# Optimization experiments

Measured on AMD Instinct MI355X. Metric: run time of the kernel, lower is better.

Reference implementation:

```python
import jax, jax.numpy as jnp
import numpy as np

NUM_HEADS = 8

def _spectral_normalize(w, u):
    # One power iteration (power_iterations=1), as in the TF wrapper.
    w2 = w.reshape(-1, w.shape[-1])            # [in, out]
    v = u @ w2.T                               # [1, in]
    v = v / jnp.linalg.norm(v)
    u_new = v @ w2                             # [1, out]
    u_new = u_new / jnp.linalg.norm(u_new)
    sigma = (v @ w2) @ u_new.T                 # [1,1]
    # TF applies normalization by variable assignment (no grad through sigma)
    return w / jax.lax.stop_gradient(sigma[0, 0])

def setup_inputs() -> dict:
    key = jax.random.key(0)
    ks = jax.random.split(key, 14)
    F = 1024
    def dense(k1, k2, k3):
        w = jax.random.normal(k1, (F, F), jnp.float32) * (1.0 / np.sqrt(F))
        b = jnp.zeros((F,), jnp.float32)
        u = jax.random.normal(k3, (1, F), jnp.float32) * 0.02
        return w, b, u
    wq, bq, uq = dense(ks[0], ks[1], ks[2])
    wk, bk, uk = dense(ks[3], ks[4], ks[5])
    wv, bv, uv = dense(ks[6], ks[7], ks[8])
    wo, bo, uo = dense(ks[9], ks[10], ks[11])
    x = jax.random.normal(ks[12], (4, 2048, F), jnp.float32)
    gamma = jnp.array(1.0, jnp.float32)
    return {"x": x, "wq": wq, "bq": bq, "uq": uq, "wk": wk, "bk": bk, "uk": uk,
            "wv": wv, "bv": bv, "uv": uv, "wo": wo, "bo": bo, "uo": uo, "gamma": gamma}

def reference(x, wq, bq, uq, wk, bk, uk, wv, bv, uv, wo, bo, uo, gamma):
    B, S, F = x.shape
    D = F // NUM_HEADS
    def proj(w, b, u):
        return x @ _spectral_normalize(w, u) + b
    def split_heads(t):
        return t.reshape(B, S, NUM_HEADS, D).transpose(0, 2, 1, 3)  # [B,H,S,D]
    q = split_heads(proj(wq, bq, uq))
    k = split_heads(proj(wk, bk, uk))
    v = split_heads(proj(wv, bv, uv))
    # NOTE: original has no 1/sqrt(depth) scaling -- faithful to source.
    logits = jnp.einsum('bhsd,bhtd->bhst', q, k)          # [B,H,S,S]
    attn = jax.nn.softmax(logits, axis=-1)
    ctx = jnp.einsum('bhst,bhtd->bhsd', attn, v)           # [B,H,S,D]
    concat = ctx.transpose(0, 2, 1, 3).reshape(B, S, F)    # merge heads
    # Dropout omitted (deterministic reference / inference mode).
    out = x + (concat @ _spectral_normalize(wo, uo) + bo) * gamma
    return (out, attn)
```

## Files before the change

kernel.cpp:

```cpp
#include <hip/hip_runtime.h>
#include <math.h>

typedef _Float16 h16;
typedef _Float16 half8 __attribute__((ext_vector_type(8)));
typedef _Float16 half4 __attribute__((ext_vector_type(4)));
typedef float floatx4 __attribute__((ext_vector_type(4)));

#define MFMA16(a, b, c) __builtin_amdgcn_mfma_f32_16x16x32_f16(a, b, c, 0, 0, 0)

__global__ void sigma_s1(const float* __restrict__ w0, const float* __restrict__ w1,
                         const float* __restrict__ w2, const float* __restrict__ w3,
                         const float* __restrict__ u0, const float* __restrict__ u1,
                         const float* __restrict__ u2, const float* __restrict__ u3,
                         float* __restrict__ tvec, float* __restrict__ acc) {
    int m = blockIdx.y;
    const float* w = (m == 0) ? w0 : (m == 1) ? w1 : (m == 2) ? w2 : w3;
    const float* u = (m == 0) ? u0 : (m == 1) ? u1 : (m == 2) ? u2 : u3;
    int wid = threadIdx.x >> 6, lane = threadIdx.x & 63;
    int row = blockIdx.x * 4 + wid;
    const float* wr = w + row * 1024;
    float s = 0.f;
    for (int k = 0; k < 16; k++) { int j = lane + 64 * k; s += u[j] * wr[j]; }
    for (int off = 32; off; off >>= 1) s += __shfl_xor(s, off, 64);
    if (lane == 0) { tvec[m * 1024 + row] = s; atomicAdd(acc + m * 2, s * s); }
}

__global__ void sigma_s2(const float* __restrict__ w0, const float* __restrict__ w1,
                         const float* __restrict__ w2, const float* __restrict__ w3,
                         const float* __restrict__ tvec, float* __restrict__ acc) {
    int m = blockIdx.y;
    const float* w = (m == 0) ? w0 : (m == 1) ? w1 : (m == 2) ? w2 : w3;
    const float* t = tvec + m * 1024;
    int j = blockIdx.x * 256 + threadIdx.x;
    float z = 0.f;
    for (int i = 0; i < 1024; i++) z += t[i] * w[i * 1024 + j];
    z = z * z;
    for (int off = 32; off; off >>= 1) z += __shfl_xor(z, off, 64);
    __shared__ float red[4];
    int wid = threadIdx.x >> 6, lane = threadIdx.x & 63;
    if (lane == 0) red[wid] = z;
    __syncthreads();
    if (threadIdx.x == 0) atomicAdd(acc + m * 2 + 1, red[0] + red[1] + red[2] + red[3]);
}

__global__ void sigma_s3(const float* __restrict__ acc, float* __restrict__ inv_sigma) {
    int m = threadIdx.x;
    if (m < 4) inv_sigma[m] = sqrtf(acc[m * 2] / acc[m * 2 + 1]);
}

__global__ void prep_w(const float* __restrict__ w, const float* __restrict__ inv_sigma,
                       int midx, h16* __restrict__ whT, h16* __restrict__ wlT) {
    __shared__ float tile[32][33];
    float is = inv_sigma[midx];
    int i0 = blockIdx.x * 32, j0 = blockIdx.y * 32;
    int tx = threadIdx.x, ty = threadIdx.y;
    for (int r = 0; r < 32; r += 8)
        tile[r + ty][tx] = w[(i0 + r + ty) * 1024 + j0 + tx] * is;
    __syncthreads();
    for (int r = 0; r < 32; r += 8) {
        int j = j0 + r + ty, i = i0 + tx;
        float v = tile[tx][r + ty];
        h16 h = (h16)v;
        whT[j * 1024 + i] = h;
        wlT[j * 1024 + i] = (h16)(v - (float)h);
    }
}

__global__ void prep_x(const float4* __restrict__ x4, half4* __restrict__ xh,
                       half4* __restrict__ xl) {
    int i = blockIdx.x * 256 + threadIdx.x;
    float4 v = x4[i];
    float a[4] = {v.x, v.y, v.z, v.w};
    half4 h, l;
    for (int k = 0; k < 4; k++) {
        h16 hh = (h16)a[k];
        h[k] = hh;
        l[k] = (h16)(a[k] - (float)hh);
    }
    xh[i] = h;
    xl[i] = l;
}

template <int SPLIT>
__global__ __launch_bounds__(256, 2) void gemm_proj(
    const h16* __restrict__ Ah_g, const h16* __restrict__ Al_g,
    const h16* __restrict__ Bh_g, const h16* __restrict__ Bl_g,
    const float* __restrict__ bias, h16* __restrict__ outh, h16* __restrict__ outl) {
    __shared__ h16 As[2][128 * 40];
    __shared__ h16 Bs[2][128 * 40];
    int tid = threadIdx.x;
    int m0 = blockIdx.y * 128, n0 = blockIdx.x * 128;
    int wid = tid >> 6, lane = tid & 63;
    int wm = (wid >> 1) * 64, wn = (wid & 1) * 64;
    int lrow = lane & 15, quad = lane >> 4;
    floatx4 acc[4][4] = {};
    for (int kt = 0; kt < 1024; kt += 32) {
        for (int i = 0; i < 2; i++) {
            int c = tid + 256 * i;
            int row = c >> 2, col = (c & 3) * 8;
            *(half8*)&As[0][row * 40 + col] = *(const half8*)&Ah_g[(m0 + row) * 1024 + kt + col];
            *(half8*)&Bs[0][row * 40 + col] = *(const half8*)&Bh_g[(n0 + row) * 1024 + kt + col];
            if (SPLIT) {
                *(half8*)&As[1][row * 40 + col] = *(const half8*)&Al_g[(m0 + row) * 1024 + kt + col];
                *(half8*)&Bs[1][row * 40 + col] = *(const half8*)&Bl_g[(n0 + row) * 1024 + kt + col];
            }
        }
        __syncthreads();
        half8 a_h[4], a_l[4], b_h[4], b_l[4];
        for (int f = 0; f < 4; f++) {
            a_h[f] = *(const half8*)&As[0][(wm + f * 16 + lrow) * 40 + quad * 8];
            b_h[f] = *(const half8*)&Bs[0][(wn + f * 16 + lrow) * 40 + quad * 8];
            if (SPLIT) {
                a_l[f] = *(const half8*)&As[1][(wm + f * 16 + lrow) * 40 + quad * 8];
                b_l[f] = *(const half8*)&Bs[1][(wn + f * 16 + lrow) * 40 + quad * 8];
            }
        }
        for (int mf = 0; mf < 4; mf++)
            for (int nf = 0; nf < 4; nf++) {
                acc[mf][nf] = MFMA16(a_h[mf], b_h[nf], acc[mf][nf]);
                if (SPLIT) {
                    acc[mf][nf] = MFMA16(a_h[mf], b_l[nf], acc[mf][nf]);
                    acc[mf][nf] = MFMA16(a_l[mf], b_h[nf], acc[mf][nf]);
                }
            }
        __syncthreads();
    }
    for (int nf = 0; nf < 4; nf++) {
        int n = n0 + wn + nf * 16 + lrow;
        float b = bias[n];
        int h = n >> 7, d = n & 127;
        for (int mf = 0; mf < 4; mf++)
            for (int r = 0; r < 4; r++) {
                int mg = m0 + wm + mf * 16 + quad * 4 + r;
                int bb = mg >> 11, s = mg & 2047;
                int idx = ((bb * 8 + h) * 2048 + s) * 128 + d;
                float v = acc[mf][nf][r] + b;
                h16 hh = (h16)v;
                outh[idx] = hh;
                if (SPLIT) outl[idx] = (h16)(v - (float)hh);
            }
    }
}

__global__ void transpose_v(const h16* __restrict__ vh, h16* __restrict__ vT) {
    __shared__ h16 tile[32][33];
    int bh = blockIdx.z;
    int t0 = blockIdx.x * 32, d0 = blockIdx.y * 32;
    int tx = threadIdx.x, ty = threadIdx.y;
    const h16* src = vh + bh * 2048 * 128;
    h16* dst = vT + bh * 128 * 2048;
    for (int r = 0; r < 32; r += 8) tile[r + ty][tx] = src[(t0 + r + ty) * 128 + d0 + tx];
    __syncthreads();
    for (int r = 0; r < 32; r += 8) dst[(d0 + r + ty) * 2048 + t0 + tx] = tile[tx][r + ty];
}

__global__ __launch_bounds__(256, 2) void gemm_logits(
    const h16* __restrict__ qh, const h16* __restrict__ ql,
    const h16* __restrict__ kh, const h16* __restrict__ kl, float* __restrict__ attn) {
    __shared__ h16 As[2][128 * 40];
    __shared__ h16 Bs[2][128 * 40];
    int tid = threadIdx.x;
    int bh = blockIdx.z;
    int s0 = blockIdx.y * 128, t0 = blockIdx.x * 128;
    const h16* Ah_g = qh + bh * 2048 * 128;
    const h16* Al_g = ql + bh * 2048 * 128;
    const h16* Bh_g = kh + bh * 2048 * 128;
    const h16* Bl_g = kl + bh * 2048 * 128;
    int wid = tid >> 6, lane = tid & 63;
    int wm = (wid >> 1) * 64, wn = (wid & 1) * 64;
    int lrow = lane & 15, quad = lane >> 4;
    floatx4 acc[4][4] = {};
    for (int kt = 0; kt < 128; kt += 32) {
        for (int i = 0; i < 2; i++) {
            int c = tid + 256 * i;
            int row = c >> 2, col = (c & 3) * 8;
            *(half8*)&As[0][row * 40 + col] = *(const half8*)&Ah_g[(s0 + row) * 128 + kt + col];
            *(half8*)&As[1][row * 40 + col] = *(const half8*)&Al_g[(s0 + row) * 128 + kt + col];
            *(half8*)&Bs[0][row * 40 + col] = *(const half8*)&Bh_g[(t0 + row) * 128 + kt + col];
            *(half8*)&Bs[1][row * 40 + col] = *(const half8*)&Bl_g[(t0 + row) * 128 + kt + col];
        }
        __syncthreads();
        half8 a_h[4], a_l[4], b_h[4], b_l[4];
        for (int f = 0; f < 4; f++) {
            a_h[f] = *(const half8*)&As[0][(wm + f * 16 + lrow) * 40 + quad * 8];
            a_l[f] = *(const half8*)&As[1][(wm + f * 16 + lrow) * 40 + quad * 8];
            b_h[f] = *(const half8*)&Bs[0][(wn + f * 16 + lrow) * 40 + quad * 8];
            b_l[f] = *(const half8*)&Bs[1][(wn + f * 16 + lrow) * 40 + quad * 8];
        }
        for (int mf = 0; mf < 4; mf++)
            for (int nf = 0; nf < 4; nf++) {
                acc[mf][nf] = MFMA16(a_h[mf], b_h[nf], acc[mf][nf]);
                acc[mf][nf] = MFMA16(a_h[mf], b_l[nf], acc[mf][nf]);
                acc[mf][nf] = MFMA16(a_l[mf], b_h[nf], acc[mf][nf]);
            }
        __syncthreads();
    }
    for (int nf = 0; nf < 4; nf++) {
        int t = t0 + wn + nf * 16 + lrow;
        for (int mf = 0; mf < 4; mf++)
            for (int r = 0; r < 4; r++) {
                int s = s0 + wm + mf * 16 + quad * 4 + r;
                attn[(bh * 2048 + s) * 2048 + t] = acc[mf][nf][r];
            }
    }
}

__global__ void row_stats(const float* __restrict__ attn, float* __restrict__ m_arr,
                          float* __restrict__ z_arr) {
    int wid = threadIdx.x >> 6, lane = threadIdx.x & 63;
    int r = blockIdx.x * 4 + wid;
    const float4* row = (const float4*)(attn + (size_t)r * 2048);
    float4 v[8];
    float mx = -1e30f;
    for (int i = 0; i < 8; i++) {
        v[i] = row[i * 64 + lane];
        mx = fmaxf(mx, fmaxf(fmaxf(v[i].x, v[i].y), fmaxf(v[i].z, v[i].w)));
    }
    for (int off = 32; off; off >>= 1) mx = fmaxf(mx, __shfl_xor(mx, off, 64));
    float z = 0.f;
    for (int i = 0; i < 8; i++)
        z += __expf(v[i].x - mx) + __expf(v[i].y - mx) + __expf(v[i].z - mx) + __expf(v[i].w - mx);
    for (int off = 32; off; off >>= 1) z += __shfl_xor(z, off, 64);
    if (lane == 0) { m_arr[r] = mx; z_arr[r] = z; }
}

__global__ __launch_bounds__(256, 2) void gemm_pv(
    float* __restrict__ attn, const h16* __restrict__ vT, const float* __restrict__ m_arr,
    const float* __restrict__ z_arr, h16* __restrict__ ctx) {
    __shared__ h16 Ps[128 * 72];
    __shared__ h16 Vs[128 * 72];
    __shared__ float ms[128], izs[128];
    int tid = threadIdx.x;
    int bh = blockIdx.y, s0 = blockIdx.x * 128;
    if (tid < 128) ms[tid] = m_arr[bh * 2048 + s0 + tid];
    else izs[tid - 128] = 1.f / z_arr[bh * 2048 + s0 + tid - 128];
    __syncthreads();
    int wid = tid >> 6, lane = tid & 63;
    int wm = (wid >> 1) * 64, wn = (wid & 1) * 64;
    int lrow = lane & 15, quad = lane >> 4;
    float* attn_b = attn + ((size_t)bh * 2048 + s0) * 2048;
    const h16* vT_b = vT + bh * 128 * 2048;
    floatx4 acc[4][4] = {};
    for (int t0 = 0; t0 < 2048; t0 += 64) {
        for (int i = 0; i < 8; i++) {
            int c = tid + 256 * i;
            int row = c >> 4, c4 = c & 15;
            float4* p = (float4*)&attn_b[(size_t)row * 2048 + t0 + c4 * 4];
            float4 l = *p;
            float mm = ms[row], iz = izs[row];
            float4 e;
            e.x = __expf(l.x - mm) * iz;
            e.y = __expf(l.y - mm) * iz;
            e.z = __expf(l.z - mm) * iz;
            e.w = __expf(l.w - mm) * iz;
            *p = e;
            half4 ph;
            ph[0] = (h16)e.x; ph[1] = (h16)e.y; ph[2] = (h16)e.z; ph[3] = (h16)e.w;
            *(half4*)&Ps[row * 72 + c4 * 4] = ph;
        }
        for (int i = 0; i < 4; i++) {
            int c = tid + 256 * i;
            int row = c >> 3, c8 = (c & 7) * 8;
            *(half8*)&Vs[row * 72 + c8] = *(const half8*)&vT_b[row * 2048 + t0 + c8];
        }
        __syncthreads();
        for (int ks = 0; ks < 2; ks++) {
            half8 a[4], b[4];
            for (int f = 0; f < 4; f++) {
                a[f] = *(const half8*)&Ps[(wm + f * 16 + lrow) * 72 + ks * 32 + quad * 8];
                b[f] = *(const half8*)&Vs[(wn + f * 16 + lrow) * 72 + ks * 32 + quad * 8];
            }
            for (int mf = 0; mf < 4; mf++)
                for (int nf = 0; nf < 4; nf++)
                    acc[mf][nf] = MFMA16(a[mf], b[nf], acc[mf][nf]);
        }
        __syncthreads();
    }
    int b = bh >> 3, h = bh & 7;
    for (int nf = 0; nf < 4; nf++) {
        int d = wn + nf * 16 + lrow;
        for (int mf = 0; mf < 4; mf++)
            for (int r = 0; r < 4; r++) {
                int s = s0 + wm + mf * 16 + quad * 4 + r;
                ctx[(b * 2048 + s) * 1024 + h * 128 + d] = (h16)acc[mf][nf][r];
            }
    }
}

__global__ __launch_bounds__(256, 2) void gemm_out(
    const h16* __restrict__ Ah_g, const h16* __restrict__ Bh_g, const float* __restrict__ bo,
    const float* __restrict__ x, const float* __restrict__ gamma_p, float* __restrict__ out) {
    __shared__ h16 As[128 * 40];
    __shared__ h16 Bs[128 * 40];
    int tid = threadIdx.x;
    int m0 = blockIdx.y * 128, n0 = blockIdx.x * 128;
    int wid = tid >> 6, lane = tid & 63;
    int wm = (wid >> 1) * 64, wn = (wid & 1) * 64;
    int lrow = lane & 15, quad = lane >> 4;
    floatx4 acc[4][4] = {};
    for (int kt = 0; kt < 1024; kt += 32) {
        for (int i = 0; i < 2; i++) {
            int c = tid + 256 * i;
            int row = c >> 2, col = (c & 3) * 8;
            *(half8*)&As[row * 40 + col] = *(const half8*)&Ah_g[(m0 + row) * 1024 + kt + col];
            *(half8*)&Bs[row * 40 + col] = *(const half8*)&Bh_g[(n0 + row) * 1024 + kt + col];
        }
        __syncthreads();
        half8 a[4], b[4];
        for (int f = 0; f < 4; f++) {
            a[f] = *(const half8*)&As[(wm + f * 16 + lrow) * 40 + quad * 8];
            b[f] = *(const half8*)&Bs[(wn + f * 16 + lrow) * 40 + quad * 8];
        }
        for (int mf = 0; mf < 4; mf++)
            for (int nf = 0; nf < 4; nf++)
                acc[mf][nf] = MFMA16(a[mf], b[nf], acc[mf][nf]);
        __syncthreads();
    }
    float g = *gamma_p;
    for (int nf = 0; nf < 4; nf++) {
        int n = n0 + wn + nf * 16 + lrow;
        float bb = bo[n];
        for (int mf = 0; mf < 4; mf++)
            for (int r = 0; r < 4; r++) {
                int mg = m0 + wm + mf * 16 + quad * 4 + r;
                out[mg * 1024 + n] = x[mg * 1024 + n] + (acc[mf][nf][r] + bb) * g;
            }
    }
}

extern "C" void kernel_launch(void* const* d_in, const int* in_sizes, int n_in,
                              void* d_out, int out_size, void* d_ws, size_t ws_size,
                              hipStream_t stream) {
    const float* x = (const float*)d_in[0];
    const float* wq = (const float*)d_in[1];
    const float* bq = (const float*)d_in[2];
    const float* uq = (const float*)d_in[3];
    const float* wk = (const float*)d_in[4];
    const float* bk = (const float*)d_in[5];
    const float* uk = (const float*)d_in[6];
    const float* wv = (const float*)d_in[7];
    const float* bv = (const float*)d_in[8];
    const float* uv = (const float*)d_in[9];
    const float* wo = (const float*)d_in[10];
    const float* bo = (const float*)d_in[11];
    const float* uo = (const float*)d_in[12];
    const float* gamma = (const float*)d_in[13];
    float* out_f = (float*)d_out;
    float* attn = out_f + 8388608;

    char* ws = (char*)d_ws;
    size_t o = 0;
    auto alloc = [&](size_t b) { size_t r = o; o += (b + 255) & ~(size_t)255; return r; };
    const size_t SZ_X = (size_t)8192 * 1024 * 2;
    const size_t SZ_W = (size_t)1024 * 1024 * 2;
    const size_t SZ_Q = (size_t)32 * 2048 * 128 * 2;
    h16* xh = (h16*)(ws + alloc(SZ_X));
    h16* xl = (h16*)(ws + alloc(SZ_X));
    h16* wqhT = (h16*)(ws + alloc(SZ_W));
    h16* wqlT = (h16*)(ws + alloc(SZ_W));
    h16* wkhT = (h16*)(ws + alloc(SZ_W));
    h16* wklT = (h16*)(ws + alloc(SZ_W));
    h16* wvhT = (h16*)(ws + alloc(SZ_W));
    h16* wvlT = (h16*)(ws + alloc(SZ_W));
    h16* wohT = (h16*)(ws + alloc(SZ_W));
    h16* wolT = (h16*)(ws + alloc(SZ_W));
    h16* qh = (h16*)(ws + alloc(SZ_Q));
    h16* ql = (h16*)(ws + alloc(SZ_Q));
    h16* kh = (h16*)(ws + alloc(SZ_Q));
    h16* kl = (h16*)(ws + alloc(SZ_Q));
    h16* vh = (h16*)(ws + alloc(SZ_Q));
    h16* vT = (h16*)(ws + alloc(SZ_Q));
    h16* ctx = (h16*)(ws + alloc(SZ_Q));
    float* tvec = (float*)(ws + alloc(4096 * 4));
    float* sacc = (float*)(ws + alloc(8 * 4));
    float* isig = (float*)(ws + alloc(4 * 4));
    float* m_arr = (float*)(ws + alloc(65536 * 4));
    float* z_arr = (float*)(ws + alloc(65536 * 4));

    (void)hipMemsetAsync(sacc, 0, 8 * 4, stream);
    sigma_s1<<<dim3(256, 4), 256, 0, stream>>>(wq, wk, wv, wo, uq, uk, uv, uo, tvec, sacc);
    sigma_s2<<<dim3(4, 4), 256, 0, stream>>>(wq, wk, wv, wo, tvec, sacc);
    sigma_s3<<<1, 64, 0, stream>>>(sacc, isig);

    prep_w<<<dim3(32, 32), dim3(32, 8), 0, stream>>>(wq, isig, 0, wqhT, wqlT);
    prep_w<<<dim3(32, 32), dim3(32, 8), 0, stream>>>(wk, isig, 1, wkhT, wklT);
    prep_w<<<dim3(32, 32), dim3(32, 8), 0, stream>>>(wv, isig, 2, wvhT, wvlT);
    prep_w<<<dim3(32, 32), dim3(32, 8), 0, stream>>>(wo, isig, 3, wohT, wolT);
    prep_x<<<8192, 256, 0, stream>>>((const float4*)x, (half4*)xh, (half4*)xl);

    gemm_proj<1><<<dim3(8, 64), 256, 0, stream>>>(xh, xl, wqhT, wqlT, bq, qh, ql);
    gemm_proj<1><<<dim3(8, 64), 256, 0, stream>>>(xh, xl, wkhT, wklT, bk, kh, kl);
    gemm_proj<0><<<dim3(8, 64), 256, 0, stream>>>(xh, xl, wvhT, wvlT, bv, vh, nullptr);
    transpose_v<<<dim3(64, 4, 32), dim3(32, 8), 0, stream>>>(vh, vT);

    gemm_logits<<<dim3(16, 16, 32), 256, 0, stream>>>(qh, ql, kh, kl, attn);
    row_stats<<<16384, 256, 0, stream>>>(attn, m_arr, z_arr);
    gemm_pv<<<dim3(16, 32), 256, 0, stream>>>(attn, vT, m_arr, z_arr, ctx);
    gemm_out<<<dim3(8, 64), 256, 0, stream>>>(ctx, wohT, bo, x, gamma, out_f);

    (void)in_sizes; (void)n_in; (void)out_size; (void)ws_size;
}
```

Baseline: 1.597 ms.

## Fuse softmax row statistics into logits GEMM and load GEMM tiles directly to LDS

The logits GEMM epilogue now computes a per-row partial max and sum-of-exponentials for each 64-column tile and writes them to scratch. A small combine kernel then merges these partials into the final row max and normaliser, replacing the separate row_stats pass that re-read the full fp32 attention matrix. Separately, all GEMM kernels switch from register-staged global-to-LDS copies to global_load_lds 16-byte direct loads. This drops the padded LDS row stride of 40, so the fragment reads may hit more LDS bank conflicts. The partial-stat buffers reuse the ctx workspace before gemm_pv writes it.

```diff
diff --git a/kernel.cpp b/kernel.cpp
--- a/kernel.cpp
+++ b/kernel.cpp
@@ -7,6 +7,11 @@
 typedef float floatx4 __attribute__((ext_vector_type(4)));
 
 #define MFMA16(a, b, c) __builtin_amdgcn_mfma_f32_16x16x32_f16(a, b, c, 0, 0, 0)
+
+__device__ __forceinline__ void gload16(const void* g, void* l) {
+    __builtin_amdgcn_global_load_lds((const __attribute__((address_space(1))) unsigned int*)g,
+                                     (__attribute__((address_space(3))) unsigned int*)l, 16, 0, 0);
+}
 
 __global__ void sigma_s1(const float* __restrict__ w0, const float* __restrict__ w1,
                          const float* __restrict__ w2, const float* __restrict__ w3,
@@ -86,33 +91,35 @@
     const h16* __restrict__ Ah_g, const h16* __restrict__ Al_g,
     const h16* __restrict__ Bh_g, const h16* __restrict__ Bl_g,
     const float* __restrict__ bias, h16* __restrict__ outh, h16* __restrict__ outl) {
-    __shared__ h16 As[2][128 * 40];
-    __shared__ h16 Bs[2][128 * 40];
+    __shared__ h16 As[2][128 * 32];
+    __shared__ h16 Bs[2][128 * 32];
     int tid = threadIdx.x;
     int m0 = blockIdx.y * 128, n0 = blockIdx.x * 128;
     int wid = tid >> 6, lane = tid & 63;
     int wm = (wid >> 1) * 64, wn = (wid & 1) * 64;
     int lrow = lane & 15, quad = lane >> 4;
+    int srow = lane >> 2;
+    int scol = (lane & 3) * 8;
     floatx4 acc[4][4] = {};
     for (int kt = 0; kt < 1024; kt += 32) {
-        for (int i = 0; i < 2; i++) {
-            int c = tid + 256 * i;
-            int row = c >> 2, col = (c & 3) * 8;
-            *(half8*)&As[0][row * 40 + col] = *(const half8*)&Ah_g[(m0 + row) * 1024 + kt + col];
-            *(half8*)&Bs[0][row * 40 + col] = *(const half8*)&Bh_g[(n0 + row) * 1024 + kt + col];
+        for (int j = 0; j < 2; j++) {
+            int rb = j * 64 + wid * 16;
+            int r = rb + srow;
+            gload16(&Ah_g[(size_t)(m0 + r) * 1024 + kt + scol], &As[0][rb * 32]);
+            gload16(&Bh_g[(size_t)(n0 + r) * 1024 + kt + scol], &Bs[0][rb * 32]);
             if (SPLIT) {
-                *(half8*)&As[1][row * 40 + col] = *(const half8*)&Al_g[(m0 + row) * 1024 + kt + col];
-                *(half8*)&Bs[1][row * 40 + col] = *(const half8*)&Bl_g[(n0 + row) * 1024 + kt + col];
+                gload16(&Al_g[(size_t)(m0 + r) * 1024 + kt + scol], &As[1][rb * 32]);
+                gload16(&Bl_g[(size_t)(n0 + r) * 1024 + kt + scol], &Bs[1][rb * 32]);
             }
         }
         __syncthreads();
         half8 a_h[4], a_l[4], b_h[4], b_l[4];
         for (int f = 0; f < 4; f++) {
-            a_h[f] = *(const half8*)&As[0][(wm + f * 16 + lrow) * 40 + quad * 8];
-            b_h[f] = *(const half8*)&Bs[0][(wn + f * 16 + lrow) * 40 + quad * 8];
+            a_h[f] = *(const half8*)&As[0][(wm + f * 16 + lrow) * 32 + quad * 8];
+            b_h[f] = *(const half8*)&Bs[0][(wn + f * 16 + lrow) * 32 + quad * 8];
             if (SPLIT) {
-                a_l[f] = *(const half8*)&As[1][(wm + f * 16 + lrow) * 40 + quad * 8];
-                b_l[f] = *(const half8*)&Bs[1][(wn + f * 16 + lrow) * 40 + quad * 8];
+                a_l[f] = *(const half8*)&As[1][(wm + f * 16 + lrow) * 32 + quad * 8];
+                b_l[f] = *(const half8*)&Bs[1][(wn + f * 16 + lrow) * 32 + quad * 8];
             }
         }
         for (int mf = 0; mf < 4; mf++)
@@ -156,9 +163,10 @@
 
 __global__ __launch_bounds__(256, 2) void gemm_logits(
     const h16* __restrict__ qh, const h16* __restrict__ ql,
-    const h16* __restrict__ kh, const h16* __restrict__ kl, float* __restrict__ attn) {
-    __shared__ h16 As[2][128 * 40];
-    __shared__ h16 Bs[2][128 * 40];
+    const h16* __restrict__ kh, const h16* __restrict__ kl, float* __restrict__ attn,
+    float* __restrict__ pmax, float* __restrict__ psum) {
+    __shared__ h16 As[2][128 * 32];
+    __shared__ h16 Bs[2][128 * 32];
     int tid = threadIdx.x;
     int bh = blockIdx.z;
     int s0 = blockIdx.y * 128, t0 = blockIdx.x * 128;
@@ -169,23 +177,25 @@
     int wid = tid >> 6, lane = tid & 63;
     int wm = (wid >> 1) * 64, wn = (wid & 1) * 64;
     int lrow = lane & 15, quad = lane >> 4;
+    int srow = lane >> 2;
+    int scol = (lane & 3) * 8;
     floatx4 acc[4][4] = {};
     for (int kt = 0; kt < 128; kt += 32) {
-        for (int i = 0; i < 2; i++) {
-            int c = tid + 256 * i;
-            int row = c >> 2, col = (c & 3) * 8;
-            *(half8*)&As[0][row * 40 + col] = *(const half8*)&Ah_g[(s0 + row) * 128 + kt + col];
-            *(half8*)&As[1][row * 40 + col] = *(const half8*)&Al_g[(s0 + row) * 128 + kt + col];
-            *(half8*)&Bs[0][row * 40 + col] = *(const half8*)&Bh_g[(t0 + row) * 128 + kt + col];
-            *(half8*)&Bs[1][row * 40 + col] = *(const half8*)&Bl_g[(t0 + row) * 128 + kt + col];
+        for (int j = 0; j < 2; j++) {
+            int rb = j * 64 + wid * 16;
+            int r = rb + srow;
+            gload16(&Ah_g[(size_t)(s0 + r) * 128 + kt + scol], &As[0][rb * 32]);
+            gload16(&Al_g[(size_t)(s0 + r) * 128 + kt + scol], &As[1][rb * 32]);
+            gload16(&Bh_g[(size_t)(t0 + r) * 128 + kt + scol], &Bs[0][rb * 32]);
+            gload16(&Bl_g[(size_t)(t0 + r) * 128 + kt + scol], &Bs[1][rb * 32]);
         }
         __syncthreads();
         half8 a_h[4], a_l[4], b_h[4], b_l[4];
         for (int f = 0; f < 4; f++) {
-            a_h[f] = *(const half8*)&As[0][(wm + f * 16 + lrow) * 40 + quad * 8];
-            a_l[f] = *(const half8*)&As[1][(wm + f * 16 + lrow) * 40 + quad * 8];
-            b_h[f] = *(const half8*)&Bs[0][(wn + f * 16 + lrow) * 40 + quad * 8];
-            b_l[f] = *(const half8*)&Bs[1][(wn + f * 16 + lrow) * 40 + quad * 8];
+            a_h[f] = *(const half8*)&As[0][(wm + f * 16 + lrow) * 32 + quad * 8];
+            a_l[f] = *(const half8*)&As[1][(wm + f * 16 + lrow) * 32 + quad * 8];
+            b_h[f] = *(const half8*)&Bs[0][(wn + f * 16 + lrow) * 32 + quad * 8];
+            b_l[f] = *(const half8*)&Bs[1][(wn + f * 16 + lrow) * 32 + quad * 8];
         }
         for (int mf = 0; mf < 4; mf++)
             for (int nf = 0; nf < 4; nf++) {
@@ -200,28 +210,37 @@
         for (int mf = 0; mf < 4; mf++)
             for (int r = 0; r < 4; r++) {
                 int s = s0 + wm + mf * 16 + quad * 4 + r;
-                attn[(bh * 2048 + s) * 2048 + t] = acc[mf][nf][r];
-            }
-    }
-}
-
-__global__ void row_stats(const float* __restrict__ attn, float* __restrict__ m_arr,
-                          float* __restrict__ z_arr) {
-    int wid = threadIdx.x >> 6, lane = threadIdx.x & 63;
-    int r = blockIdx.x * 4 + wid;
-    const float4* row = (const float4*)(attn + (size_t)r * 2048);
-    float4 v[8];
-    float mx = -1e30f;
-    for (int i = 0; i < 8; i++) {
-        v[i] = row[i * 64 + lane];
-        mx = fmaxf(mx, fmaxf(fmaxf(v[i].x, v[i].y), fmaxf(v[i].z, v[i].w)));
-    }
-    for (int off = 32; off; off >>= 1) mx = fmaxf(mx, __shfl_xor(mx, off, 64));
+                attn[((size_t)bh * 2048 + s) * 2048 + t] = acc[mf][nf][r];
+            }
+    }
+    int tile = blockIdx.x * 2 + (wid & 1);
+    for (int mf = 0; mf < 4; mf++)
+        for (int r = 0; r < 4; r++) {
+            float mx = fmaxf(fmaxf(acc[mf][0][r], acc[mf][1][r]),
+                             fmaxf(acc[mf][2][r], acc[mf][3][r]));
+            for (int off = 8; off; off >>= 1) mx = fmaxf(mx, __shfl_xor(mx, off, 64));
+            float z = __expf(acc[mf][0][r] - mx) + __expf(acc[mf][1][r] - mx) +
+                      __expf(acc[mf][2][r] - mx) + __expf(acc[mf][3][r] - mx);
+            for (int off = 8; off; off >>= 1) z += __shfl_xor(z, off, 64);
+            if (lrow == 0) {
+                int s = s0 + wm + mf * 16 + quad * 4 + r;
+                pmax[((size_t)bh * 2048 + s) * 32 + tile] = mx;
+                psum[((size_t)bh * 2048 + s) * 32 + tile] = z;
+            }
+        }
+}
+
+__global__ void combine_stats(const float* __restrict__ pmax, const float* __restrict__ psum,
+                              float* __restrict__ m_arr, float* __restrict__ z_arr) {
+    int r = blockIdx.x * 256 + threadIdx.x;
+    const float* pm = pmax + (size_t)r * 32;
+    const float* ps = psum + (size_t)r * 32;
+    float m = -1e30f;
+    for (int i = 0; i < 32; i++) m = fmaxf(m, pm[i]);
     float z = 0.f;
-    for (int i = 0; i < 8; i++)
-        z += __expf(v[i].x - mx) + __expf(v[i].y - mx) + __expf(v[i].z - mx) + __expf(v[i].w - mx);
-    for (int off = 32; off; off >>= 1) z += __shfl_xor(z, off, 64);
-    if (lane == 0) { m_arr[r] = mx; z_arr[r] = z; }
+    for (int i = 0; i < 32; i++) z += ps[i] * __expf(pm[i] - m);
+    m_arr[r] = m;
+    z_arr[r] = z;
 }
 
 __global__ __launch_bounds__(256, 2) void gemm_pv(
@@ -290,26 +309,28 @@
 __global__ __launch_bounds__(256, 2) void gemm_out(
     const h16* __restrict__ Ah_g, const h16* __restrict__ Bh_g, const float* __restrict__ bo,
     const float* __restrict__ x, const float* __restrict__ gamma_p, float* __restrict__ out) {
-    __shared__ h16 As[128 * 40];
-    __shared__ h16 Bs[128 * 40];
+    __shared__ h16 As[128 * 32];
+    __shared__ h16 Bs[128 * 32];
     int tid = threadIdx.x;
     int m0 = blockIdx.y * 128, n0 = blockIdx.x * 128;
     int wid = tid >> 6, lane = tid & 63;
     int wm = (wid >> 1) * 64, wn = (wid & 1) * 64;
     int lrow = lane & 15, quad = lane >> 4;
+    int srow = lane >> 2;
+    int scol = (lane & 3) * 8;
     floatx4 acc[4][4] = {};
     for (int kt = 0; kt < 1024; kt += 32) {
-        for (int i = 0; i < 2; i++) {
-            int c = tid + 256 * i;
-            int row = c >> 2, col = (c & 3) * 8;
-            *(half8*)&As[row * 40 + col] = *(const half8*)&Ah_g[(m0 + row) * 1024 + kt + col];
-            *(half8*)&Bs[row * 40 + col] = *(const half8*)&Bh_g[(n0 + row) * 1024 + kt + col];
+        for (int j = 0; j < 2; j++) {
+            int rb = j * 64 + wid * 16;
+            int r = rb + srow;
+            gload16(&Ah_g[(size_t)(m0 + r) * 1024 + kt + scol], &As[rb * 32]);
+            gload16(&Bh_g[(size_t)(n0 + r) * 1024 + kt + scol], &Bs[rb * 32]);
         }
         __syncthreads();
         half8 a[4], b[4];
         for (int f = 0; f < 4; f++) {
-            a[f] = *(const half8*)&As[(wm + f * 16 + lrow) * 40 + quad * 8];
-            b[f] = *(const half8*)&Bs[(wn + f * 16 + lrow) * 40 + quad * 8];
+            a[f] = *(const half8*)&As[(wm + f * 16 + lrow) * 32 + quad * 8];
+            b[f] = *(const half8*)&Bs[(wn + f * 16 + lrow) * 32 + quad * 8];
         }
         for (int mf = 0; mf < 4; mf++)
             for (int nf = 0; nf < 4; nf++)
@@ -376,6 +397,8 @@
     float* isig = (float*)(ws + alloc(4 * 4));
     float* m_arr = (float*)(ws + alloc(65536 * 4));
     float* z_arr = (float*)(ws + alloc(65536 * 4));
+    float* pmax = (float*)ctx;
+    float* psum = pmax + (size_t)65536 * 32;
 
     (void)hipMemsetAsync(sacc, 0, 8 * 4, stream);
     sigma_s1<<<dim3(256, 4), 256, 0, stream>>>(wq, wk, wv, wo, uq, uk, uv, uo, tvec, sacc);
@@ -393,8 +416,8 @@
     gemm_proj<0><<<dim3(8, 64), 256, 0, stream>>>(xh, xl, wvhT, wvlT, bv, vh, nullptr);
     transpose_v<<<dim3(64, 4, 32), dim3(32, 8), 0, stream>>>(vh, vT);
 
-    gemm_logits<<<dim3(16, 16, 32), 256, 0, stream>>>(qh, ql, kh, kl, attn);
-    row_stats<<<16384, 256, 0, stream>>>(attn, m_arr, z_arr);
+    gemm_logits<<<dim3(16, 16, 32), 256, 0, stream>>>(qh, ql, kh, kl, attn, pmax, psum);
+    combine_stats<<<256, 256, 0, stream>>>(pmax, psum, m_arr, z_arr);
     gemm_pv<<<dim3(16, 32), 256, 0, stream>>>(attn, vT, m_arr, z_arr, ctx);
     gemm_out<<<dim3(8, 64), 256, 0, stream>>>(ctx, wohT, bo, x, gamma, out_f);
 
```

New measurement: 1.467 ms. 1.09x faster.
